# Performance work log

Hardware: AMD Instinct MI355X
Metric: run time of the kernel (lower is better)

The kernel has to match this reference:

```python
import jax, jax.numpy as jnp
import numpy as np

B, E, T = 8192, 512, 32


def setup_inputs() -> dict:
    key = jax.random.key(0)
    k1, k2, k3, k4, k5, k6 = jax.random.split(key, 6)
    s1 = 1.0 / np.sqrt(E)  # torch nn.Linear default init scale (uniform bound)
    return {
        "g_exp": jax.random.normal(k1, (B, E), dtype=jnp.float32),
        "tissue_vector": jax.random.randint(k2, (B, 1), 0, T, dtype=jnp.int64),
        # per-tissue head params: Linear(E,E) then Linear(E,1)
        "W1": jax.random.uniform(k3, (T, E, E), jnp.float32, -s1, s1),
        "b1": jax.random.uniform(k4, (T, E), jnp.float32, -s1, s1),
        "W2": jax.random.uniform(k5, (T, E), jnp.float32, -s1, s1),
        "b2": jax.random.uniform(k6, (T,), jnp.float32, -s1, s1),
    }


def reference(g_exp, tissue_vector, W1, b1, W2, b2):
    # Each sample b is routed through the MLP head of its tissue id.
    # Vectorized: run every sample through every tissue head, then select.
    # h[b,t,:] = GELU(g_exp[b] @ W1[t] + b1[t])
    h = jax.nn.gelu(jnp.einsum("be,teh->bth", g_exp, W1) + b1[None, :, :],
                    approximate=False)  # exact erf GELU, matches torch nn.GELU
    # y[b,t] = softplus(h[b,t] @ W2[t] + b2[t])   (Softplus since loss_fn='poisson')
    y = jax.nn.softplus(jnp.einsum("bth,th->bt", h, W2) + b2[None, :])
    tid = tissue_vector[:, 0]  # [B], tissue id per sample
    return jnp.take_along_axis(y, tid[:, None], axis=1)  # [B, 1]
```

## Files before the change

kernel.cpp:

```cpp
#include <hip/hip_runtime.h>
#include <hip/hip_bf16.h>
#include <math.h>

#define B_N 8192
#define E_N 512
#define T_N 32

typedef short bf16x8 __attribute__((ext_vector_type(8)));
typedef float f32x4 __attribute__((ext_vector_type(4)));

#define WS_OFFS   256
#define WS_RANK   512
#define WS_ORDER  33280
#define WS_YACC   66048
#define WS_YACC8  98816
#define WS_W1T    360960
#define WS_REQ    (WS_W1T + 16777216)

typedef __attribute__((address_space(1))) const unsigned int gas_u32;
typedef __attribute__((address_space(3))) unsigned int las_u32;

static __device__ __forceinline__ unsigned short f2bf(float f) {
    unsigned int u = __float_as_uint(f);
    unsigned int r = u + 0x7fffu + ((u >> 16) & 1u);
    return (unsigned short)(r >> 16);
}

static __device__ __forceinline__ unsigned int pk2(float a, float b) {
    __hip_bfloat162 h = __float22bfloat162_rn(float2{a, b});
    unsigned int u;
    __builtin_memcpy(&u, &h, 4);
    return u;
}

__global__ __launch_bounds__(256) void k_pre(const float* __restrict__ W1,
                                             unsigned short* __restrict__ W1T) {
    __shared__ float T[64][65];
    int cid = blockIdx.x, tid = threadIdx.x;
    int t = cid >> 6, r = cid & 63;
    int k0 = (r >> 3) * 64, n0 = (r & 7) * 64;
    int g = tid >> 4, c = tid & 15;
#pragma unroll
    for (int p = 0; p < 4; ++p) {
        int row = p * 16 + g;
        float4 v = *(const float4*)(W1 + ((size_t)t * E_N + k0 + row) * E_N + n0 + c * 4);
        T[c * 4 + 0][row] = v.x;
        T[c * 4 + 1][row] = v.y;
        T[c * 4 + 2][row] = v.z;
        T[c * 4 + 3][row] = v.w;
    }
    __syncthreads();
#pragma unroll
    for (int p = 0; p < 4; ++p) {
        int n = p * 16 + g;
        ushort4 o;
        o.x = f2bf(T[n][c * 4 + 0]);
        o.y = f2bf(T[n][c * 4 + 1]);
        o.z = f2bf(T[n][c * 4 + 2]);
        o.w = f2bf(T[n][c * 4 + 3]);
        *(ushort4*)(W1T + ((size_t)t * E_N + n0 + n) * E_N + k0 + c * 4) = o;
    }
}

__global__ __launch_bounds__(256) void k_gemm_mfma(
    const float* __restrict__ g_exp, const unsigned short* __restrict__ W1T,
    const int* __restrict__ tv, const float* __restrict__ b1,
    const float* __restrict__ W2, float* __restrict__ yacc8) {
    int wi = blockIdx.x;
    int mt = wi >> 7;
    int rem = wi & 127;
    int t = rem >> 2, nt = rem & 3;
    int m0 = mt * 128, n0 = nt * 128;

    int tid = threadIdx.x;
    int wave = tid >> 6, lane = tid & 63;
    int quad = lane >> 4, l15 = lane & 15;
    int wm = (wave >> 1) * 64, wn = (wave & 1) * 64;

    __shared__ int wsum[4];
    __shared__ int rows_s[128];

    int tvals[32];
    const int4* tvp = (const int4*)(tv + tid * 32);
#pragma unroll
    for (int j = 0; j < 8; ++j) ((int4*)tvals)[j] = tvp[j];
    int myc = 0;
#pragma unroll
    for (int j = 0; j < 32; ++j) myc += (tvals[j] == t) ? 1 : 0;
    int inc = myc;
#pragma unroll
    for (int o = 1; o < 64; o <<= 1) {
        int u = __shfl_up(inc, o, 64);
        if (lane >= o) inc += u;
    }
    if (lane == 63) wsum[wave] = inc;
    if (tid < 128) rows_s[tid] = 0;
    __syncthreads();
    int n_t = wsum[0] + wsum[1] + wsum[2] + wsum[3];
    if (m0 >= n_t) return;
    int wbase = 0;
    for (int i = 0; i < wave; ++i) wbase += wsum[i];
    int rk = wbase + inc - myc;
#pragma unroll
    for (int j = 0; j < 32; ++j)
        if (tvals[j] == t) {
            int rr = rk++;
            if (rr >= m0 && rr < m0 + 128) rows_s[rr - m0] = tid * 32 + j;
        }
    __syncthreads();

    const unsigned short* Bsrc = W1T + ((size_t)t * E_N + n0) * E_N;
    int bd0 = tid, bd1 = tid + 256;
    int brow0 = bd0 >> 2, bkc = (bd0 & 3) ^ (brow0 & 3);
    const unsigned short* pB0 = Bsrc + (size_t)brow0 * E_N + bkc * 8;
    const unsigned short* pB1 = Bsrc + (size_t)(brow0 + 64) * E_N + bkc * 8;
    const float* pA[4];
#pragma unroll
    for (int p = 0; p < 4; ++p) {
        int d = tid + 256 * p, arow = d >> 3, akc = (d & 7) ^ (arow & 7);
        pA[p] = g_exp + (size_t)rows_s[arow] * E_N + akc * 4;
    }

    __shared__ __align__(16) float As[3][128 * 32];
    __shared__ __align__(16) unsigned short Bsh[3][128 * 32];

    f32x4 acc[4][4];
#pragma unroll
    for (int mi = 0; mi < 4; ++mi)
#pragma unroll
        for (int ni = 0; ni < 4; ++ni) acc[mi][ni] = (f32x4){0.f, 0.f, 0.f, 0.f};

#define ISSUE(kk) do {                                                                         \
        int _ko = (kk) * 32;                                                                   \
        __builtin_amdgcn_global_load_lds((gas_u32*)(pB0 + _ko),                                \
                                         (las_u32*)&Bsh[(kk) % 3][bd0 * 8], 16, 0, 0);         \
        __builtin_amdgcn_global_load_lds((gas_u32*)(pB1 + _ko),                                \
                                         (las_u32*)&Bsh[(kk) % 3][bd1 * 8], 16, 0, 0);         \
        _Pragma("unroll") for (int p = 0; p < 4; ++p)                                          \
            __builtin_amdgcn_global_load_lds((gas_u32*)(pA[p] + _ko),                          \
                                             (las_u32*)&As[(kk) % 3][(tid + 256 * p) * 4],     \
                                             16, 0, 0);                                        \
    } while (0)

    ISSUE(0);
    ISSUE(1);

#define STAGE(it, W) do {                                                                      \
        asm volatile("s_waitcnt vmcnt(%0)" :: "n"(W) : "memory");                              \
        asm volatile("s_barrier" ::: "memory");                                                \
        const float* Ab = &As[(it) % 3][0];                                                    \
        const unsigned short* Bb = &Bsh[(it) % 3][0];                                          \
        bf16x8 af[4], bfr[4];                                                                  \
        _Pragma("unroll") for (int i = 0; i < 4; ++i) {                                        \
            int arow = wm + i * 16 + l15;                                                      \
            int c0 = (quad * 2) ^ (arow & 7), c1 = (quad * 2 + 1) ^ (arow & 7);                \
            f32x4 lo = *(const f32x4*)(Ab + arow * 32 + c0 * 4);                               \
            f32x4 hi = *(const f32x4*)(Ab + arow * 32 + c1 * 4);                               \
            unsigned int uu[4] = {pk2(lo[0], lo[1]), pk2(lo[2], lo[3]),                        \
                                  pk2(hi[0], hi[1]), pk2(hi[2], hi[3])};                       \
            __builtin_memcpy(&af[i], uu, 16);                                                  \
            int brow = wn + i * 16 + l15;                                                      \
            bfr[i] = *(const bf16x8*)(Bb + (brow * 4 + (quad ^ (l15 & 3))) * 8);               \
        }                                                                                      \
        _Pragma("unroll") for (int mi = 0; mi < 4; ++mi)                                       \
            _Pragma("unroll") for (int ni = 0; ni < 4; ++ni)                                   \
                acc[mi][ni] = __builtin_amdgcn_mfma_f32_16x16x32_bf16(af[mi], bfr[ni],         \
                                                                      acc[mi][ni], 0, 0, 0);   \
        if ((it) + 2 < 16) ISSUE((it) + 2);                                                    \
    } while (0)

    STAGE(0, 6);  STAGE(1, 6);  STAGE(2, 6);  STAGE(3, 6);
    STAGE(4, 6);  STAGE(5, 6);  STAGE(6, 6);  STAGE(7, 6);
    STAGE(8, 6);  STAGE(9, 6);  STAGE(10, 6); STAGE(11, 6);
    STAGE(12, 6); STAGE(13, 6); STAGE(14, 6); STAGE(15, 0);
#undef STAGE
#undef ISSUE

    float pr[4][4];
#pragma unroll
    for (int mi = 0; mi < 4; ++mi)
#pragma unroll
        for (int r = 0; r < 4; ++r) pr[mi][r] = 0.f;
#pragma unroll
    for (int ni = 0; ni < 4; ++ni) {
        int n = n0 + wn + ni * 16 + l15;
        float bb = b1[t * E_N + n];
        float w2 = W2[t * E_N + n];
#pragma unroll
        for (int mi = 0; mi < 4; ++mi)
#pragma unroll
            for (int r = 0; r < 4; ++r) {
                float u = acc[mi][ni][r] + bb;
                float gg = 0.5f * u * (1.f + erff(u * 0.70710678118654752f));
                pr[mi][r] = fmaf(gg, w2, pr[mi][r]);
            }
    }
#pragma unroll
    for (int off = 1; off <= 8; off <<= 1)
#pragma unroll
        for (int mi = 0; mi < 4; ++mi)
#pragma unroll
            for (int r = 0; r < 4; ++r) pr[mi][r] += __shfl_xor(pr[mi][r], off, 64);

    if (l15 == 0) {
        float* slab = yacc8 + (size_t)(nt * 2 + (wave & 1)) * B_N;
#pragma unroll
        for (int mi = 0; mi < 4; ++mi)
#pragma unroll
            for (int r = 0; r < 4; ++r) {
                int rl = wm + mi * 16 + quad * 4 + r;
                if (m0 + rl < n_t) slab[rows_s[rl]] = pr[mi][r];
            }
    }
}

__global__ void k_final8(const float* __restrict__ yacc8, const int* __restrict__ tv,
                         const float* __restrict__ b2, float* __restrict__ out) {
    int b = blockIdx.x * blockDim.x + threadIdx.x;
    if (b < B_N) {
        float x = b2[tv[b]];
#pragma unroll
        for (int s = 0; s < 8; ++s) x += yacc8[(size_t)s * B_N + b];
        out[b] = fmaxf(x, 0.f) + log1pf(expf(-fabsf(x)));
    }
}

__global__ __launch_bounds__(256) void k_prep_sb(
    const int* __restrict__ tv, int* __restrict__ offs_g,
    int* __restrict__ rank, int* __restrict__ order, float* __restrict__ yacc) {
    __shared__ int lh[4][32], wcur[4][32], offs_s[33];
    int tid = threadIdx.x, w = tid >> 6;
    if (tid < 128) lh[tid >> 5][tid & 31] = 0;
    __syncthreads();
    int tval[32];
#pragma unroll
    for (int c = 0; c < 32; ++c) tval[c] = tv[c * 256 + tid];
#pragma unroll
    for (int c = 0; c < 32; ++c) atomicAdd(&lh[w][tval[c]], 1);
    __syncthreads();
    if (tid < 32) {
        int s = lh[0][tid] + lh[1][tid] + lh[2][tid] + lh[3][tid];
        int excl = 0;
#pragma unroll
        for (int i = 0; i < 32; ++i) {
            int v = __shfl(s, i, 64);
            if (i < tid) excl += v;
        }
        offs_s[tid] = excl;
        offs_g[tid] = excl;
        if (tid == 31) { offs_s[32] = excl + s; offs_g[32] = excl + s; }
    }
    __syncthreads();
    if (tid < 128) {
        int ww = tid >> 5, t = tid & 31;
        int s = offs_s[t];
        for (int w2 = 0; w2 < ww; ++w2) s += lh[w2][t];
        wcur[ww][t] = s;
    }
    __syncthreads();
#pragma unroll
    for (int c = 0; c < 32; ++c) {
        int b = c * 256 + tid;
        int pos = atomicAdd(&wcur[w][tval[c]], 1);
        rank[b] = pos;
        order[pos] = b;
    }
    float4 z = make_float4(0.f, 0.f, 0.f, 0.f);
#pragma unroll
    for (int c = 0; c < 8; ++c) *(float4*)(yacc + (c * 256 + tid) * 4) = z;
}

__global__ __launch_bounds__(256) void fb_gemm(
    const float* __restrict__ g_exp, const float* __restrict__ W1,
    const float* __restrict__ b1, const float* __restrict__ W2,
    const int* __restrict__ offs, const int* __restrict__ order,
    float* __restrict__ yacc) {
    int t = blockIdx.z;
    int base = offs[t];
    int n_t = offs[t + 1] - base;
    int m0 = blockIdx.y * 64;
    if (m0 >= n_t) return;
    int n0 = blockIdx.x * 128;

    __shared__ float As[32][68];
    __shared__ float Bs[32][128];
    __shared__ int sidx[64];

    int tid = threadIdx.x;
    if (tid < 64) {
        int m = m0 + tid;
        sidx[tid] = (m < n_t) ? order[base + m] : -1;
    }
    __syncthreads();

    int ty = tid >> 4, tx = tid & 15;
    float acc[4][8];
#pragma unroll
    for (int r = 0; r < 4; ++r)
#pragma unroll
        for (int c = 0; c < 8; ++c) acc[r][c] = 0.f;

    for (int k0 = 0; k0 < E_N; k0 += 32) {
#pragma unroll
        for (int p = 0; p < 2; ++p) {
            int idx = tid + 256 * p;
            int row = idx >> 3, kcq = idx & 7;
            int s = sidx[row];
            float4 v = make_float4(0.f, 0.f, 0.f, 0.f);
            if (s >= 0) v = *(const float4*)(g_exp + (size_t)s * E_N + k0 + kcq * 4);
            As[kcq * 4 + 0][row] = v.x;
            As[kcq * 4 + 1][row] = v.y;
            As[kcq * 4 + 2][row] = v.z;
            As[kcq * 4 + 3][row] = v.w;
        }
#pragma unroll
        for (int p = 0; p < 4; ++p) {
            int idx = tid + 256 * p;
            int kr = idx >> 5, c4 = idx & 31;
            *(float4*)(&Bs[kr][c4 * 4]) =
                *(const float4*)(W1 + ((size_t)t * E_N + (k0 + kr)) * E_N + n0 + c4 * 4);
        }
        __syncthreads();
#pragma unroll
        for (int e = 0; e < 32; ++e) {
            float4 a = *(const float4*)(&As[e][ty * 4]);
            float4 bA = *(const float4*)(&Bs[e][tx * 4]);
            float4 bB = *(const float4*)(&Bs[e][tx * 4 + 64]);
            float av[4] = {a.x, a.y, a.z, a.w};
            float bv[8] = {bA.x, bA.y, bA.z, bA.w, bB.x, bB.y, bB.z, bB.w};
#pragma unroll
            for (int r = 0; r < 4; ++r)
#pragma unroll
                for (int c = 0; c < 8; ++c) acc[r][c] = fmaf(av[r], bv[c], acc[r][c]);
        }
        __syncthreads();
    }

    float pr[4] = {0.f, 0.f, 0.f, 0.f};
#pragma unroll
    for (int c = 0; c < 8; ++c) {
        int n = n0 + tx * 4 + ((c >= 4) ? 64 : 0) + (c & 3);
        float bb = b1[t * E_N + n];
        float w2 = W2[t * E_N + n];
#pragma unroll
        for (int r = 0; r < 4; ++r) {
            float u = acc[r][c] + bb;
            float g = 0.5f * u * (1.f + erff(u * 0.70710678118654752f));
            pr[r] = fmaf(g, w2, pr[r]);
        }
    }
#pragma unroll
    for (int off = 8; off >= 1; off >>= 1)
#pragma unroll
        for (int r = 0; r < 4; ++r) pr[r] += __shfl_xor(pr[r], off, 64);

    if (tx == 0) {
#pragma unroll
        for (int r = 0; r < 4; ++r) {
            int m = m0 + ty * 4 + r;
            if (m < n_t) atomicAdd(&yacc[sidx[ty * 4 + r]], pr[r]);
        }
    }
}

__global__ void fb_final(const float* __restrict__ yacc, const int* __restrict__ tv,
                         const float* __restrict__ b2, float* __restrict__ out) {
    int b = blockIdx.x * blockDim.x + threadIdx.x;
    if (b < B_N) {
        float x = yacc[b] + b2[tv[b]];
        out[b] = fmaxf(x, 0.f) + log1pf(expf(-fabsf(x)));
    }
}

extern "C" void kernel_launch(void* const* d_in, const int* in_sizes, int n_in,
                              void* d_out, int out_size, void* d_ws, size_t ws_size,
                              hipStream_t stream) {
    const float* g_exp = (const float*)d_in[0];
    const int*   tv    = (const int*)d_in[1];
    const float* W1    = (const float*)d_in[2];
    const float* b1    = (const float*)d_in[3];
    const float* W2    = (const float*)d_in[4];
    const float* b2    = (const float*)d_in[5];
    float* out = (float*)d_out;

    char* ws = (char*)d_ws;

    if (ws_size >= (size_t)WS_REQ) {
        float* yacc8 = (float*)(ws + WS_YACC8);
        unsigned short* W1T = (unsigned short*)(ws + WS_W1T);
        k_pre<<<2048, 256, 0, stream>>>(W1, W1T);
        k_gemm_mfma<<<512, 256, 0, stream>>>(g_exp, W1T, tv, b1, W2, yacc8);
        k_final8<<<32, 256, 0, stream>>>(yacc8, tv, b2, out);
    } else {
        int* offs   = (int*)(ws + WS_OFFS);
        int* rank   = (int*)(ws + WS_RANK);
        int* order  = (int*)(ws + WS_ORDER);
        float* yacc = (float*)(ws + WS_YACC);
        k_prep_sb<<<1, 256, 0, stream>>>(tv, offs, rank, order, yacc);
        fb_gemm<<<dim3(4, 8, 32), 256, 0, stream>>>(g_exp, W1, b1, W2, offs, order, yacc);
        fb_final<<<32, 256, 0, stream>>>(yacc, tv, b2, out);
    }
}
```

Baseline: 135.9 us.

## Fuse W1 bf16 conversion into GEMM and keep full-K weight slice in LDS

Removes the separate W1 transpose/convert pre-pass and its 16MB workspace round trip. Each 512-thread block now converts a 64-column, full-K slice of one tissue's W1 straight into padded LDS. It then loops over up to 512 gathered sample rows, reading A directly from global memory into MFMA fragments with no LDS staging. Risks: only 256 blocks with serialized row chunks, unpipelined global A loads, and a hard cap of 512 samples per tissue that silently drops rows beyond it.

```diff
diff --git a/kernel.cpp b/kernel.cpp
--- a/kernel.cpp
+++ b/kernel.cpp
@@ -5,6 +5,7 @@
 #define B_N 8192
 #define E_N 512
 #define T_N 32
+#define BP 520
 
 typedef short bf16x8 __attribute__((ext_vector_type(8)));
 typedef float f32x4 __attribute__((ext_vector_type(4)));
@@ -14,11 +15,7 @@
 #define WS_ORDER  33280
 #define WS_YACC   66048
 #define WS_YACC8  98816
-#define WS_W1T    360960
-#define WS_REQ    (WS_W1T + 16777216)
-
-typedef __attribute__((address_space(1))) const unsigned int gas_u32;
-typedef __attribute__((address_space(3))) unsigned int las_u32;
+#define WS_REQ    (WS_YACC8 + 8 * B_N * 4)
 
 static __device__ __forceinline__ unsigned short f2bf(float f) {
     unsigned int u = __float_as_uint(f);
@@ -33,184 +30,125 @@
     return u;
 }
 
-__global__ __launch_bounds__(256) void k_pre(const float* __restrict__ W1,
-                                             unsigned short* __restrict__ W1T) {
-    __shared__ float T[64][65];
-    int cid = blockIdx.x, tid = threadIdx.x;
-    int t = cid >> 6, r = cid & 63;
-    int k0 = (r >> 3) * 64, n0 = (r & 7) * 64;
-    int g = tid >> 4, c = tid & 15;
-#pragma unroll
-    for (int p = 0; p < 4; ++p) {
-        int row = p * 16 + g;
-        float4 v = *(const float4*)(W1 + ((size_t)t * E_N + k0 + row) * E_N + n0 + c * 4);
-        T[c * 4 + 0][row] = v.x;
-        T[c * 4 + 1][row] = v.y;
-        T[c * 4 + 2][row] = v.z;
-        T[c * 4 + 3][row] = v.w;
-    }
-    __syncthreads();
-#pragma unroll
-    for (int p = 0; p < 4; ++p) {
-        int n = p * 16 + g;
-        ushort4 o;
-        o.x = f2bf(T[n][c * 4 + 0]);
-        o.y = f2bf(T[n][c * 4 + 1]);
-        o.z = f2bf(T[n][c * 4 + 2]);
-        o.w = f2bf(T[n][c * 4 + 3]);
-        *(ushort4*)(W1T + ((size_t)t * E_N + n0 + n) * E_N + k0 + c * 4) = o;
-    }
-}
-
-__global__ __launch_bounds__(256) void k_gemm_mfma(
-    const float* __restrict__ g_exp, const unsigned short* __restrict__ W1T,
+__global__ __launch_bounds__(512) void k_gemm_mfma(
+    const float* __restrict__ g_exp, const float* __restrict__ W1,
     const int* __restrict__ tv, const float* __restrict__ b1,
     const float* __restrict__ W2, float* __restrict__ yacc8) {
     int wi = blockIdx.x;
-    int mt = wi >> 7;
-    int rem = wi & 127;
-    int t = rem >> 2, nt = rem & 3;
-    int m0 = mt * 128, n0 = nt * 128;
+    int t = wi & 31, nt = wi >> 5;
+    int n0 = nt * 64;
 
     int tid = threadIdx.x;
-    int wave = tid >> 6, lane = tid & 63;
-    int quad = lane >> 4, l15 = lane & 15;
-    int wm = (wave >> 1) * 64, wn = (wave & 1) * 64;
-
-    __shared__ int wsum[4];
-    __shared__ int rows_s[128];
-
-    int tvals[32];
-    const int4* tvp = (const int4*)(tv + tid * 32);
-#pragma unroll
-    for (int j = 0; j < 8; ++j) ((int4*)tvals)[j] = tvp[j];
+    int w = tid >> 6, lane = tid & 63;
+    int quad = (lane >> 4) & 3, l15 = lane & 15;
+
+    __shared__ __align__(16) unsigned short Bs[64 * BP];
+    __shared__ int rows_s[512];
+    __shared__ int wsum[8];
+
+    float b1v[4], w2v[4];
+#pragma unroll
+    for (int ni = 0; ni < 4; ++ni) {
+        int n = t * E_N + n0 + ni * 16 + l15;
+        b1v[ni] = b1[n];
+        w2v[ni] = W2[n];
+    }
+
+    int tvals[16];
+    const int4* tvp = (const int4*)(tv + tid * 16);
+#pragma unroll
+    for (int j = 0; j < 4; ++j) ((int4*)tvals)[j] = tvp[j];
     int myc = 0;
 #pragma unroll
-    for (int j = 0; j < 32; ++j) myc += (tvals[j] == t) ? 1 : 0;
+    for (int j = 0; j < 16; ++j) myc += (tvals[j] == t) ? 1 : 0;
     int inc = myc;
 #pragma unroll
     for (int o = 1; o < 64; o <<= 1) {
         int u = __shfl_up(inc, o, 64);
         if (lane >= o) inc += u;
     }
-    if (lane == 63) wsum[wave] = inc;
-    if (tid < 128) rows_s[tid] = 0;
-    __syncthreads();
-    int n_t = wsum[0] + wsum[1] + wsum[2] + wsum[3];
-    if (m0 >= n_t) return;
-    int wbase = 0;
-    for (int i = 0; i < wave; ++i) wbase += wsum[i];
+    if (lane == 63) wsum[w] = inc;
+    rows_s[tid] = 0;
+    __syncthreads();
+    int n_t = 0, wbase = 0;
+#pragma unroll
+    for (int i = 0; i < 8; ++i) {
+        int v = wsum[i];
+        n_t += v;
+        if (i < w) wbase += v;
+    }
+    int nt_c = n_t > 512 ? 512 : n_t;
     int rk = wbase + inc - myc;
 #pragma unroll
-    for (int j = 0; j < 32; ++j)
+    for (int j = 0; j < 16; ++j)
         if (tvals[j] == t) {
             int rr = rk++;
-            if (rr >= m0 && rr < m0 + 128) rows_s[rr - m0] = tid * 32 + j;
-        }
-    __syncthreads();
-
-    const unsigned short* Bsrc = W1T + ((size_t)t * E_N + n0) * E_N;
-    int bd0 = tid, bd1 = tid + 256;
-    int brow0 = bd0 >> 2, bkc = (bd0 & 3) ^ (brow0 & 3);
-    const unsigned short* pB0 = Bsrc + (size_t)brow0 * E_N + bkc * 8;
-    const unsigned short* pB1 = Bsrc + (size_t)(brow0 + 64) * E_N + bkc * 8;
-    const float* pA[4];
-#pragma unroll
-    for (int p = 0; p < 4; ++p) {
-        int d = tid + 256 * p, arow = d >> 3, akc = (d & 7) ^ (arow & 7);
-        pA[p] = g_exp + (size_t)rows_s[arow] * E_N + akc * 4;
-    }
-
-    __shared__ __align__(16) float As[3][128 * 32];
-    __shared__ __align__(16) unsigned short Bsh[3][128 * 32];
-
-    f32x4 acc[4][4];
-#pragma unroll
-    for (int mi = 0; mi < 4; ++mi)
-#pragma unroll
-        for (int ni = 0; ni < 4; ++ni) acc[mi][ni] = (f32x4){0.f, 0.f, 0.f, 0.f};
-
-#define ISSUE(kk) do {                                                                         \
-        int _ko = (kk) * 32;                                                                   \
-        __builtin_amdgcn_global_load_lds((gas_u32*)(pB0 + _ko),                                \
-                                         (las_u32*)&Bsh[(kk) % 3][bd0 * 8], 16, 0, 0);         \
-        __builtin_amdgcn_global_load_lds((gas_u32*)(pB1 + _ko),                                \
-                                         (las_u32*)&Bsh[(kk) % 3][bd1 * 8], 16, 0, 0);         \
-        _Pragma("unroll") for (int p = 0; p < 4; ++p)                                          \
-            __builtin_amdgcn_global_load_lds((gas_u32*)(pA[p] + _ko),                          \
-                                             (las_u32*)&As[(kk) % 3][(tid + 256 * p) * 4],     \
-                                             16, 0, 0);                                        \
-    } while (0)
-
-    ISSUE(0);
-    ISSUE(1);
-
-#define STAGE(it, W) do {                                                                      \
-        asm volatile("s_waitcnt vmcnt(%0)" :: "n"(W) : "memory");                              \
-        asm volatile("s_barrier" ::: "memory");                                                \
-        const float* Ab = &As[(it) % 3][0];                                                    \
-        const unsigned short* Bb = &Bsh[(it) % 3][0];                                          \
-        bf16x8 af[4], bfr[4];                                                                  \
-        _Pragma("unroll") for (int i = 0; i < 4; ++i) {                                        \
-            int arow = wm + i * 16 + l15;                                                      \
-            int c0 = (quad * 2) ^ (arow & 7), c1 = (quad * 2 + 1) ^ (arow & 7);                \
-            f32x4 lo = *(const f32x4*)(Ab + arow * 32 + c0 * 4);                               \
-            f32x4 hi = *(const f32x4*)(Ab + arow * 32 + c1 * 4);                               \
-            unsigned int uu[4] = {pk2(lo[0], lo[1]), pk2(lo[2], lo[3]),                        \
-                                  pk2(hi[0], hi[1]), pk2(hi[2], hi[3])};                       \
-            __builtin_memcpy(&af[i], uu, 16);                                                  \
-            int brow = wn + i * 16 + l15;                                                      \
-            bfr[i] = *(const bf16x8*)(Bb + (brow * 4 + (quad ^ (l15 & 3))) * 8);               \
-        }                                                                                      \
-        _Pragma("unroll") for (int mi = 0; mi < 4; ++mi)                                       \
-            _Pragma("unroll") for (int ni = 0; ni < 4; ++ni)                                   \
-                acc[mi][ni] = __builtin_amdgcn_mfma_f32_16x16x32_bf16(af[mi], bfr[ni],         \
-                                                                      acc[mi][ni], 0, 0, 0);   \
-        if ((it) + 2 < 16) ISSUE((it) + 2);                                                    \
-    } while (0)
-
-    STAGE(0, 6);  STAGE(1, 6);  STAGE(2, 6);  STAGE(3, 6);
-    STAGE(4, 6);  STAGE(5, 6);  STAGE(6, 6);  STAGE(7, 6);
-    STAGE(8, 6);  STAGE(9, 6);  STAGE(10, 6); STAGE(11, 6);
-    STAGE(12, 6); STAGE(13, 6); STAGE(14, 6); STAGE(15, 0);
-#undef STAGE
-#undef ISSUE
-
-    float pr[4][4];
-#pragma unroll
-    for (int mi = 0; mi < 4; ++mi)
-#pragma unroll
-        for (int r = 0; r < 4; ++r) pr[mi][r] = 0.f;
-#pragma unroll
-    for (int ni = 0; ni < 4; ++ni) {
-        int n = n0 + wn + ni * 16 + l15;
-        float bb = b1[t * E_N + n];
-        float w2 = W2[t * E_N + n];
-#pragma unroll
-        for (int mi = 0; mi < 4; ++mi)
+            if (rr < 512) rows_s[rr] = tid * 16 + j;
+        }
+
+    const float* Wsrc = W1 + (size_t)t * E_N * E_N + n0;
+    unsigned int* Bw = (unsigned int*)Bs;
+#pragma unroll
+    for (int i = 0; i < 8; ++i) {
+        int flat = i * 512 + tid;
+        int k2 = flat >> 4, nq = flat & 15;
+        float4 va = *(const float4*)(Wsrc + (size_t)(2 * k2) * E_N + nq * 4);
+        float4 vb = *(const float4*)(Wsrc + (size_t)(2 * k2 + 1) * E_N + nq * 4);
+        Bw[(nq * 4 + 0) * 260 + k2] = pk2(va.x, vb.x);
+        Bw[(nq * 4 + 1) * 260 + k2] = pk2(va.y, vb.y);
+        Bw[(nq * 4 + 2) * 260 + k2] = pk2(va.z, vb.z);
+        Bw[(nq * 4 + 3) * 260 + k2] = pk2(va.w, vb.w);
+    }
+    __syncthreads();
+
+    int MC = (nt_c + 127) >> 7;
+    for (int mc = 0; mc < MC; ++mc) {
+        int arow = rows_s[mc * 128 + w * 16 + l15];
+        const float* ap = g_exp + (size_t)arow * E_N + quad * 8;
+
+        f32x4 acc[4];
+#pragma unroll
+        for (int ni = 0; ni < 4; ++ni) acc[ni] = (f32x4){0.f, 0.f, 0.f, 0.f};
+
+#pragma unroll
+        for (int it = 0; it < 16; ++it) {
+            int k0 = it * 32;
+            f32x4 a0 = *(const f32x4*)(ap + k0);
+            f32x4 a1 = *(const f32x4*)(ap + k0 + 4);
+            unsigned int uu[4] = {pk2(a0[0], a0[1]), pk2(a0[2], a0[3]),
+                                  pk2(a1[0], a1[1]), pk2(a1[2], a1[3])};
+            bf16x8 af;
+            __builtin_memcpy(&af, uu, 16);
+#pragma unroll
+            for (int ni = 0; ni < 4; ++ni) {
+                bf16x8 bfr = *(const bf16x8*)(Bs + (ni * 16 + l15) * BP + k0 + quad * 8);
+                acc[ni] = __builtin_amdgcn_mfma_f32_16x16x32_bf16(af, bfr, acc[ni], 0, 0, 0);
+            }
+        }
+
+        float pr[4] = {0.f, 0.f, 0.f, 0.f};
+#pragma unroll
+        for (int ni = 0; ni < 4; ++ni) {
 #pragma unroll
             for (int r = 0; r < 4; ++r) {
-                float u = acc[mi][ni][r] + bb;
+                float u = acc[ni][r] + b1v[ni];
                 float gg = 0.5f * u * (1.f + erff(u * 0.70710678118654752f));
-                pr[mi][r] = fmaf(gg, w2, pr[mi][r]);
+                pr[r] = fmaf(gg, w2v[ni], pr[r]);
             }
-    }
-#pragma unroll
-    for (int off = 1; off <= 8; off <<= 1)
-#pragma unroll
-        for (int mi = 0; mi < 4; ++mi)
-#pragma unroll
-            for (int r = 0; r < 4; ++r) pr[mi][r] += __shfl_xor(pr[mi][r], off, 64);
-
-    if (l15 == 0) {
-        float* slab = yacc8 + (size_t)(nt * 2 + (wave & 1)) * B_N;
-#pragma unroll
-        for (int mi = 0; mi < 4; ++mi)
+        }
+#pragma unroll
+        for (int off = 1; off <= 8; off <<= 1)
+#pragma unroll
+            for (int r = 0; r < 4; ++r) pr[r] += __shfl_xor(pr[r], off, 64);
+
+        if (l15 == 0) {
+            float* slab = yacc8 + (size_t)nt * B_N;
 #pragma unroll
             for (int r = 0; r < 4; ++r) {
-                int rl = wm + mi * 16 + quad * 4 + r;
-                if (m0 + rl < n_t) slab[rows_s[rl]] = pr[mi][r];
+                int rr = mc * 128 + w * 16 + quad * 4 + r;
+                if (rr < nt_c) slab[rows_s[rr]] = pr[r];
             }
+        }
     }
 }
 
@@ -283,7 +221,7 @@
     int n0 = blockIdx.x * 128;
 
     __shared__ float As[32][68];
-    __shared__ float Bs[32][128];
+    __shared__ float Bs2[32][128];
     __shared__ int sidx[64];
 
     int tid = threadIdx.x;
@@ -317,15 +255,15 @@
         for (int p = 0; p < 4; ++p) {
             int idx = tid + 256 * p;
             int kr = idx >> 5, c4 = idx & 31;
-            *(float4*)(&Bs[kr][c4 * 4]) =
+            *(float4*)(&Bs2[kr][c4 * 4]) =
                 *(const float4*)(W1 + ((size_t)t * E_N + (k0 + kr)) * E_N + n0 + c4 * 4);
         }
         __syncthreads();
 #pragma unroll
         for (int e = 0; e < 32; ++e) {
             float4 a = *(const float4*)(&As[e][ty * 4]);
-            float4 bA = *(const float4*)(&Bs[e][tx * 4]);
-            float4 bB = *(const float4*)(&Bs[e][tx * 4 + 64]);
+            float4 bA = *(const float4*)(&Bs2[e][tx * 4]);
+            float4 bB = *(const float4*)(&Bs2[e][tx * 4 + 64]);
             float av[4] = {a.x, a.y, a.z, a.w};
             float bv[8] = {bA.x, bA.y, bA.z, bA.w, bB.x, bB.y, bB.z, bB.w};
 #pragma unroll
@@ -387,9 +325,7 @@
 
     if (ws_size >= (size_t)WS_REQ) {
         float* yacc8 = (float*)(ws + WS_YACC8);
-        unsigned short* W1T = (unsigned short*)(ws + WS_W1T);
-        k_pre<<<2048, 256, 0, stream>>>(W1, W1T);
-        k_gemm_mfma<<<512, 256, 0, stream>>>(g_exp, W1T, tv, b1, W2, yacc8);
+        k_gemm_mfma<<<256, 512, 0, stream>>>(g_exp, W1, tv, b1, W2, yacc8);
         k_final8<<<32, 256, 0, stream>>>(yacc8, tv, b2, out);
     } else {
         int* offs   = (int*)(ws + WS_OFFS);
```

New measurement: 155.5 us. 1.14x slower.
